# Performance work log

Measured on AMD Instinct MI355X. Metric: run time of the kernel, lower is better.

Reference implementation:

```python
import jax, jax.numpy as jnp
import numpy as np
import math

HIDDEN = 768
LABEL_NUM = 16
N_HEADS = 12
HEAD_DIM = HIDDEN // N_HEADS


def setup_inputs() -> dict:
    key = jax.random.key(0)
    ks = jax.random.split(key, 8)
    B, S, L, Ls, H = 8, 128, LABEL_NUM, 8, HIDDEN
    std = 1.0 / math.sqrt(H)
    return {
        "token_embs": jax.random.normal(ks[0], (B, S, H), jnp.float32),
        "label_embs": jax.random.normal(ks[1], (L, Ls, H), jnp.float32),
        "token_mask": jnp.ones((B, S), jnp.float32),
        "label_mask": jnp.ones((L, Ls), jnp.float32),
        "Wq": jax.random.normal(ks[2], (H, H), jnp.float32) * std,
        "bq": jnp.zeros((H,), jnp.float32),
        "Wk": jax.random.normal(ks[3], (H, H), jnp.float32) * std,
        "bk": jnp.zeros((H,), jnp.float32),
        "Wv": jax.random.normal(ks[4], (H, H), jnp.float32) * std,
        "bv": jnp.zeros((H,), jnp.float32),
    }


def reference(token_embs, label_embs, token_mask, label_mask, Wq, bq, Wk, bk, Wv, bv):
    B, S, H = token_embs.shape
    L, Ls, _ = label_embs.shape
    T = S + Ls
    # broadcast (instead of repeat) then concat: [B, L, T, H] -> [B*L, T, H]
    tok = jnp.broadcast_to(token_embs[:, None, :, :], (B, L, S, H))
    lab = jnp.broadcast_to(label_embs[None, :, :, :], (B, L, Ls, H))
    x = jnp.concatenate([tok, lab], axis=2).reshape(B * L, T, H)
    # mask: [B*L, T]; extended additive mask (1-m)*-10000
    tm = jnp.broadcast_to(token_mask[:, None, :], (B, L, S))
    lm = jnp.broadcast_to(label_mask[None, :, :], (B, L, Ls))
    mask = jnp.concatenate([tm, lm], axis=2).reshape(B * L, T)
    bias = (1.0 - mask) * -10000.0  # [BL, T]
    # QKV (torch Linear: y = x W^T + b)
    q = (x @ Wq.T + bq).reshape(B * L, T, N_HEADS, HEAD_DIM)
    k = (x @ Wk.T + bk).reshape(B * L, T, N_HEADS, HEAD_DIM)
    v = (x @ Wv.T + bv).reshape(B * L, T, N_HEADS, HEAD_DIM)
    scores = jnp.einsum("bthd,bshd->bhts", q, k) / math.sqrt(HEAD_DIM)
    scores = scores + bias[:, None, None, :]
    probs = jax.nn.softmax(scores, axis=-1)
    ctx = jnp.einsum("bhts,bshd->bthd", probs, v).reshape(B * L, T, H)
    # [B, L, T, H] -> [B, T, L, H]
    fused = ctx.reshape(B, L, T, H).transpose(0, 2, 1, 3)
    return (fused,)
```

## Files before the change

kernel.cpp:

```cpp
#include <hip/hip_runtime.h>
#include <hip/hip_bf16.h>
#include <stdint.h>

#define HIDDEN 768
#define NH 12
#define HD 64
#define BB 8
#define SS 128
#define LL 16
#define LS 8
#define TT 136
#define NROWS 1152
#define BH (BB * NH)

typedef __attribute__((ext_vector_type(8))) short bf16x8;
typedef __attribute__((ext_vector_type(4))) float f32x4;
typedef __hip_bfloat16 bf16;

__device__ inline float tof(bf16 x) { return __bfloat162float(x); }
__device__ inline uint16_t b16bits(float f) {
    bf16 h = __float2bfloat16(f);
    union { bf16 h; uint16_t u; } u; u.h = h; return u.u;
}

__global__ __launch_bounds__(256) void qkv_kernel(
    const float* __restrict__ tok, const float* __restrict__ lab,
    const float* __restrict__ Wq, const float* __restrict__ bq,
    const float* __restrict__ Wk, const float* __restrict__ bk,
    const float* __restrict__ Wv, const float* __restrict__ bv,
    bf16* __restrict__ Qw, bf16* __restrict__ Kw, bf16* __restrict__ Vw)
{
    __shared__ __align__(16) uint16_t As[64 * 40];
    __shared__ __align__(16) uint16_t Bs[128 * 40];

    int tid = threadIdx.x;
    int lane = tid & 63, wv = tid >> 6;
    int ml = lane & 15, quad = lane >> 4;
    int mt = blockIdx.x / 18, nt = blockIdx.x % 18;
    int wr = wv >> 1, wc = wv & 1;

    int mat = nt / 6;
    int col0 = (nt % 6) * 128;
    const float* wbase = (mat == 0) ? Wq : ((mat == 1) ? Wk : Wv);
    const float* bptr  = (mat == 0) ? bq : ((mat == 1) ? bk : bv);
    bf16* obase        = (mat == 0) ? Qw : ((mat == 1) ? Kw : Vw);

    int ar0 = mt * 64;
    const float* asrc = (ar0 < 1024) ? (tok + (size_t)ar0 * HIDDEN)
                                     : (lab + (size_t)(ar0 - 1024) * HIDDEN);
    const float* bsrc = wbase + (size_t)col0 * HIDDEN;

    f32x4 acc[2][4] = {};

    for (int k0 = 0; k0 < HIDDEN; k0 += 32) {
        #pragma unroll
        for (int i = 0; i < 2; ++i) {
            int gi = i * 256 + tid;
            int r = gi >> 3, kc = (gi & 7) * 4;
            float4 v = *reinterpret_cast<const float4*>(asrc + (size_t)r * HIDDEN + k0 + kc);
            ushort4 hh;
            hh.x = b16bits(v.x); hh.y = b16bits(v.y);
            hh.z = b16bits(v.z); hh.w = b16bits(v.w);
            *reinterpret_cast<ushort4*>(&As[r * 40 + kc]) = hh;
        }
        #pragma unroll
        for (int i = 0; i < 4; ++i) {
            int gi = i * 256 + tid;
            int r = gi >> 3, kc = (gi & 7) * 4;
            float4 v = *reinterpret_cast<const float4*>(bsrc + (size_t)r * HIDDEN + k0 + kc);
            ushort4 hh;
            hh.x = b16bits(v.x); hh.y = b16bits(v.y);
            hh.z = b16bits(v.z); hh.w = b16bits(v.w);
            *reinterpret_cast<ushort4*>(&Bs[r * 40 + kc]) = hh;
        }
        __syncthreads();

        bf16x8 af[2], bfr[4];
        #pragma unroll
        for (int rt = 0; rt < 2; ++rt)
            af[rt] = *reinterpret_cast<const bf16x8*>(&As[(wr * 32 + rt * 16 + ml) * 40 + quad * 8]);
        #pragma unroll
        for (int ct = 0; ct < 4; ++ct)
            bfr[ct] = *reinterpret_cast<const bf16x8*>(&Bs[(wc * 64 + ct * 16 + ml) * 40 + quad * 8]);
        #pragma unroll
        for (int rt = 0; rt < 2; ++rt)
            #pragma unroll
            for (int ct = 0; ct < 4; ++ct)
                acc[rt][ct] = __builtin_amdgcn_mfma_f32_16x16x32_bf16(af[rt], bfr[ct], acc[rt][ct], 0, 0, 0);
        __syncthreads();
    }

    #pragma unroll
    for (int ct = 0; ct < 4; ++ct) {
        int c = col0 + wc * 64 + ct * 16 + ml;
        float bvv = bptr[c];
        #pragma unroll
        for (int rt = 0; rt < 2; ++rt) {
            #pragma unroll
            for (int reg = 0; reg < 4; ++reg) {
                int R = mt * 64 + wr * 32 + rt * 16 + quad * 4 + reg;
                obase[(size_t)R * HIDDEN + c] = __float2bfloat16(acc[rt][ct][reg] + bvv);
            }
        }
    }
}

__global__ __launch_bounds__(256) void attn_tt_kernel(
    const bf16* __restrict__ Qw, const bf16* __restrict__ Kw,
    const bf16* __restrict__ Vw, const float* __restrict__ tmask,
    bf16* __restrict__ ctx_tt, float* __restrict__ m_tt, float* __restrict__ d_tt)
{
    __shared__ __align__(16) uint32_t KldsW[128 * 36];
    __shared__ __align__(16) uint32_t VtW[64 * 68];
    __shared__ __align__(16) uint32_t PW[4][16 * 68];
    __shared__ float bias_s[128];

    int bh = blockIdx.x >> 1;
    int hf = blockIdx.x & 1;
    int b = bh / NH, h = bh % NH;
    int tid = threadIdx.x;
    int lane = tid & 63, wv = tid >> 6;
    int ml = lane & 15, quad = lane >> 4;

    for (int i = tid; i < 128 * 32; i += 256) {
        int s = i >> 5, w = i & 31;
        KldsW[s * 36 + w] =
            reinterpret_cast<const uint32_t*>(Kw + (size_t)(b * SS + s) * HIDDEN + h * HD)[w];
    }
    for (int i = tid; i < 64 * 64; i += 256) {
        int d = i & 63, s2 = i >> 6;
        const uint16_t* v0 = reinterpret_cast<const uint16_t*>(Vw + (size_t)(b * SS + 2 * s2) * HIDDEN + h * HD);
        const uint16_t* v1 = reinterpret_cast<const uint16_t*>(Vw + (size_t)(b * SS + 2 * s2 + 1) * HIDDEN + h * HD);
        VtW[d * 68 + s2] = (uint32_t)v0[d] | ((uint32_t)v1[d] << 16);
    }
    for (int i = tid; i < 128; i += 256)
        bias_s[i] = (1.0f - tmask[b * SS + i]) * -10000.0f;
    __syncthreads();

    const bf16* Klb = reinterpret_cast<const bf16*>(KldsW);
    const bf16* Vtb = reinterpret_cast<const bf16*>(VtW);
    const bf16* Pb  = reinterpret_cast<const bf16*>(PW[wv]);

    int qr = hf * 64 + wv * 16 + ml;
    const bf16* qp = Qw + (size_t)(b * SS + qr) * HIDDEN + h * HD + quad * 8;
    bf16x8 a0 = *reinterpret_cast<const bf16x8*>(qp);
    bf16x8 a1 = *reinterpret_cast<const bf16x8*>(qp + 32);

    f32x4 sc[8];
    #pragma unroll
    for (int ct = 0; ct < 8; ++ct) {
        const bf16* kp = Klb + (ct * 16 + ml) * 72 + quad * 8;
        bf16x8 b0 = *reinterpret_cast<const bf16x8*>(kp);
        bf16x8 b1 = *reinterpret_cast<const bf16x8*>(kp + 32);
        f32x4 z = {0.f, 0.f, 0.f, 0.f};
        z = __builtin_amdgcn_mfma_f32_16x16x32_bf16(a0, b0, z, 0, 0, 0);
        z = __builtin_amdgcn_mfma_f32_16x16x32_bf16(a1, b1, z, 0, 0, 0);
        sc[ct] = z;
    }

    float mx[4] = {-1e30f, -1e30f, -1e30f, -1e30f};
    #pragma unroll
    for (int ct = 0; ct < 8; ++ct) {
        float bc = bias_s[ct * 16 + ml];
        #pragma unroll
        for (int reg = 0; reg < 4; ++reg) {
            float v = sc[ct][reg] * 0.125f + bc;
            sc[ct][reg] = v;
            mx[reg] = fmaxf(mx[reg], v);
        }
    }
    #pragma unroll
    for (int reg = 0; reg < 4; ++reg)
        #pragma unroll
        for (int off = 1; off < 16; off <<= 1)
            mx[reg] = fmaxf(mx[reg], __shfl_xor(mx[reg], off));

    float Zs[4] = {0.f, 0.f, 0.f, 0.f};
    #pragma unroll
    for (int ct = 0; ct < 8; ++ct) {
        #pragma unroll
        for (int reg = 0; reg < 4; ++reg) {
            float e = __expf(sc[ct][reg] - mx[reg]);
            sc[ct][reg] = e;
            Zs[reg] += e;
        }
    }
    #pragma unroll
    for (int reg = 0; reg < 4; ++reg)
        #pragma unroll
        for (int off = 1; off < 16; off <<= 1)
            Zs[reg] += __shfl_xor(Zs[reg], off);

    #pragma unroll
    for (int reg = 0; reg < 4; ++reg) {
        int gr = bh * 128 + hf * 64 + wv * 16 + quad * 4 + reg;
        if (ml == 0) { m_tt[gr] = mx[reg]; d_tt[gr] = Zs[reg]; }
    }

    #pragma unroll
    for (int ct = 0; ct < 8; ++ct) {
        #pragma unroll
        for (int reg = 0; reg < 4; ++reg) {
            float e = sc[ct][reg];
            float ep = __shfl_xor(e, 1);
            if ((ml & 1) == 0)
                PW[wv][(quad * 4 + reg) * 68 + ct * 8 + (ml >> 1)] =
                    (uint32_t)b16bits(e) | ((uint32_t)b16bits(ep) << 16);
        }
    }

    float rZ[4];
    #pragma unroll
    for (int reg = 0; reg < 4; ++reg) rZ[reg] = 1.0f / Zs[reg];

    #pragma unroll
    for (int ct4 = 0; ct4 < 4; ++ct4) {
        f32x4 acc = {0.f, 0.f, 0.f, 0.f};
        #pragma unroll
        for (int ks = 0; ks < 4; ++ks) {
            bf16x8 ap = *reinterpret_cast<const bf16x8*>(Pb + ml * 136 + ks * 32 + quad * 8);
            bf16x8 bp = *reinterpret_cast<const bf16x8*>(Vtb + (ct4 * 16 + ml) * 136 + ks * 32 + quad * 8);
            acc = __builtin_amdgcn_mfma_f32_16x16x32_bf16(ap, bp, acc, 0, 0, 0);
        }
        #pragma unroll
        for (int reg = 0; reg < 4; ++reg) {
            int gr = bh * 128 + hf * 64 + wv * 16 + quad * 4 + reg;
            ctx_tt[(size_t)gr * 64 + ct4 * 16 + ml] = __float2bfloat16(acc[reg] * rZ[reg]);
        }
    }
}

__global__ __launch_bounds__(256) void attn_merge_kernel(
    const bf16* __restrict__ Qw, const bf16* __restrict__ Kw,
    const bf16* __restrict__ Vw,
    const bf16* __restrict__ ctx_tt, const float* __restrict__ m_tt,
    const float* __restrict__ d_tt,
    const float* __restrict__ tmask, const float* __restrict__ lmask,
    float* __restrict__ out)
{
    __shared__ __align__(16) uint32_t VtW[64 * 84];
    __shared__ __align__(16) uint32_t PW[4][16 * 84];
    __shared__ float mtt_s[128], dtt_s[128], bias_t[128];
    __shared__ float bias_l[16];

    int p = blockIdx.x & 7;
    int h = (blockIdx.x >> 3) % NH;
    int b = blockIdx.x / (8 * NH);
    int l0 = 2 * p, l1 = l0 + 1;
    int bh = b * NH + h;
    int tid = threadIdx.x;
    int lane = tid & 63, wv = tid >> 6;
    int ml = lane & 15, quad = lane >> 4;

    for (int i = tid; i < 64 * 80; i += 256) {
        int d = i & 63, s2 = i >> 6;
        uint32_t w = 0;
        #pragma unroll
        for (int half = 0; half < 2; ++half) {
            int s = 2 * s2 + half;
            int row = -1;
            if (s < 128)      row = b * SS + s;
            else if (s < 136) row = 1024 + l0 * LS + (s - 128);
            else if (s < 144) row = 1024 + l1 * LS + (s - 136);
            uint16_t v = 0;
            if (row >= 0)
                v = reinterpret_cast<const uint16_t*>(Vw + (size_t)row * HIDDEN + h * HD)[d];
            w |= (uint32_t)v << (16 * half);
        }
        VtW[d * 84 + s2] = w;
    }
    if (tid < 128) {
        mtt_s[tid] = m_tt[bh * 128 + tid];
        dtt_s[tid] = d_tt[bh * 128 + tid];
        bias_t[tid] = (1.0f - tmask[b * SS + tid]) * -10000.0f;
    }
    if (tid < 16) {
        int labk = (tid < 8) ? (l0 * LS + tid) : (l1 * LS + tid - 8);
        bias_l[tid] = (1.0f - lmask[labk]) * -10000.0f;
    }
    for (int i = tid; i < 4 * 16 * 8; i += 256) {
        int wvb = i >> 7, rem = i & 127;
        PW[wvb][(rem >> 3) * 84 + 72 + (rem & 7)] = 0;
    }
    __syncthreads();

    const bf16* Vtb = reinterpret_cast<const bf16*>(VtW);
    const bf16* Pb  = reinterpret_cast<const bf16*>(PW[wv]);
    const bf16x8 zfrag = {0, 0, 0, 0, 0, 0, 0, 0};

    int kprow = 1024 + ((ml < 8) ? (l0 * LS + ml) : (l1 * LS + ml - 8));
    const bf16* kpp = Kw + (size_t)kprow * HIDDEN + h * HD + quad * 8;
    bf16x8 kb0 = *reinterpret_cast<const bf16x8*>(kpp);
    bf16x8 kb1 = *reinterpret_cast<const bf16x8*>(kpp + 32);

    for (int rt = wv; rt < 8; rt += 4) {
        int tq = rt * 16 + ml;
        const bf16* qp = Qw + (size_t)(b * SS + tq) * HIDDEN + h * HD + quad * 8;
        bf16x8 a0 = *reinterpret_cast<const bf16x8*>(qp);
        bf16x8 a1 = *reinterpret_cast<const bf16x8*>(qp + 32);

        f32x4 z = {0.f, 0.f, 0.f, 0.f};
        z = __builtin_amdgcn_mfma_f32_16x16x32_bf16(a0, kb0, z, 0, 0, 0);
        z = __builtin_amdgcn_mfma_f32_16x16x32_bf16(a1, kb1, z, 0, 0, 0);

        float w0r[4], i0r[4], w1r[4], i1r[4];
        #pragma unroll
        for (int reg = 0; reg < 4; ++reg) {
            int grow = rt * 16 + quad * 4 + reg;
            float s = z[reg] * 0.125f + bias_l[ml];
            float m = s;
            m = fmaxf(m, __shfl_xor(m, 1));
            m = fmaxf(m, __shfl_xor(m, 2));
            m = fmaxf(m, __shfl_xor(m, 4));
            float mtt = mtt_s[grow], dtt = dtt_s[grow];
            float m_new = fmaxf(mtt, m);
            float e = __expf(s - m_new);
            float dh = e;
            dh += __shfl_xor(dh, 1);
            dh += __shfl_xor(dh, 2);
            dh += __shfl_xor(dh, 4);
            float alpha = __expf(mtt - m_new);
            float w = alpha * dtt;
            float inv = 1.0f / (w + dh);
            w0r[reg] = __shfl(w,   (lane & 48));
            i0r[reg] = __shfl(inv, (lane & 48));
            w1r[reg] = __shfl(w,   (lane & 48) | 8);
            i1r[reg] = __shfl(inv, (lane & 48) | 8);
            float ep = __shfl_xor(e, 1);
            if ((ml & 1) == 0)
                PW[wv][(quad * 4 + reg) * 84 + (ml >> 1)] =
                    (uint32_t)b16bits(e) | ((uint32_t)b16bits(ep) << 16);
        }

        bf16x8 aP0 = (quad == 0) ? *reinterpret_cast<const bf16x8*>(Pb + ml * 168)     : zfrag;
        bf16x8 aP1 = (quad == 0) ? *reinterpret_cast<const bf16x8*>(Pb + ml * 168 + 8) : zfrag;
        #pragma unroll
        for (int ct4 = 0; ct4 < 4; ++ct4) {
            const bf16* vrow = Vtb + (ct4 * 16 + ml) * 168;
            bf16x8 bV0 = (quad == 0) ? *reinterpret_cast<const bf16x8*>(vrow + 128) : zfrag;
            bf16x8 bV1 = (quad == 0) ? *reinterpret_cast<const bf16x8*>(vrow + 136) : zfrag;
            f32x4 pv0 = {0.f, 0.f, 0.f, 0.f}, pv1 = {0.f, 0.f, 0.f, 0.f};
            pv0 = __builtin_amdgcn_mfma_f32_16x16x32_bf16(aP0, bV0, pv0, 0, 0, 0);
            pv1 = __builtin_amdgcn_mfma_f32_16x16x32_bf16(aP1, bV1, pv1, 0, 0, 0);
            #pragma unroll
            for (int reg = 0; reg < 4; ++reg) {
                int grow = rt * 16 + quad * 4 + reg;
                float c = tof(ctx_tt[(size_t)(bh * 128 + grow) * 64 + ct4 * 16 + ml]);
                size_t ob = (((size_t)b * TT + grow) * LL) * HIDDEN + h * HD + ct4 * 16 + ml;
                out[ob + (size_t)l0 * HIDDEN] = (w0r[reg] * c + pv0[reg]) * i0r[reg];
                out[ob + (size_t)l1 * HIDDEN] = (w1r[reg] * c + pv1[reg]) * i1r[reg];
            }
        }
    }

    if (wv == 3) {
        int qrow = 1024 + ((ml < 8) ? (l0 * LS + ml) : (l1 * LS + ml - 8));
        const bf16* qp = Qw + (size_t)qrow * HIDDEN + h * HD + quad * 8;
        bf16x8 a0 = *reinterpret_cast<const bf16x8*>(qp);
        bf16x8 a1 = *reinterpret_cast<const bf16x8*>(qp + 32);

        f32x4 sc[9];
        #pragma unroll
        for (int ct = 0; ct < 9; ++ct) {
            bf16x8 b0, b1;
            if (ct < 8) {
                const bf16* kp = Kw + (size_t)(b * SS + ct * 16 + ml) * HIDDEN + h * HD + quad * 8;
                b0 = *reinterpret_cast<const bf16x8*>(kp);
                b1 = *reinterpret_cast<const bf16x8*>(kp + 32);
            } else { b0 = kb0; b1 = kb1; }
            f32x4 zz = {0.f, 0.f, 0.f, 0.f};
            zz = __builtin_amdgcn_mfma_f32_16x16x32_bf16(a0, b0, zz, 0, 0, 0);
            zz = __builtin_amdgcn_mfma_f32_16x16x32_bf16(a1, b1, zz, 0, 0, 0);
            sc[ct] = zz;
        }

        float mx[4] = {-1e30f, -1e30f, -1e30f, -1e30f};
        #pragma unroll
        for (int ct = 0; ct < 9; ++ct) {
            #pragma unroll
            for (int reg = 0; reg < 4; ++reg) {
                int rq = quad * 4 + reg;
                float bc = (ct < 8) ? bias_t[ct * 16 + ml]
                                    : (((rq < 8) != (ml < 8)) ? -1e30f : bias_l[ml]);
                float v = sc[ct][reg] * 0.125f + bc;
                sc[ct][reg] = v;
                mx[reg] = fmaxf(mx[reg], v);
            }
        }
        #pragma unroll
        for (int reg = 0; reg < 4; ++reg)
            #pragma unroll
            for (int off = 1; off < 16; off <<= 1)
                mx[reg] = fmaxf(mx[reg], __shfl_xor(mx[reg], off));

        float Zs[4] = {0.f, 0.f, 0.f, 0.f};
        #pragma unroll
        for (int ct = 0; ct < 9; ++ct) {
            #pragma unroll
            for (int reg = 0; reg < 4; ++reg) {
                float e = __expf(sc[ct][reg] - mx[reg]);
                sc[ct][reg] = e;
                Zs[reg] += e;
            }
        }
        #pragma unroll
        for (int reg = 0; reg < 4; ++reg)
            #pragma unroll
            for (int off = 1; off < 16; off <<= 1)
                Zs[reg] += __shfl_xor(Zs[reg], off);
        float zi[4];
        #pragma unroll
        for (int reg = 0; reg < 4; ++reg) zi[reg] = 1.0f / Zs[reg];

        #pragma unroll
        for (int ct = 0; ct < 9; ++ct) {
            #pragma unroll
            for (int reg = 0; reg < 4; ++reg) {
                float e = sc[ct][reg];
                float ep = __shfl_xor(e, 1);
                if ((ml & 1) == 0)
                    PW[wv][(quad * 4 + reg) * 84 + ct * 8 + (ml >> 1)] =
                        (uint32_t)b16bits(e) | ((uint32_t)b16bits(ep) << 16);
            }
        }

        #pragma unroll
        for (int ct4 = 0; ct4 < 4; ++ct4) {
            f32x4 acc = {0.f, 0.f, 0.f, 0.f};
            #pragma unroll
            for (int ks = 0; ks < 5; ++ks) {
                bf16x8 ap = *reinterpret_cast<const bf16x8*>(Pb + ml * 168 + ks * 32 + quad * 8);
                bf16x8 bp = *reinterpret_cast<const bf16x8*>(Vtb + (ct4 * 16 + ml) * 168 + ks * 32 + quad * 8);
                acc = __builtin_amdgcn_mfma_f32_16x16x32_bf16(ap, bp, acc, 0, 0, 0);
            }
            #pragma unroll
            for (int reg = 0; reg < 4; ++reg) {
                int rq = quad * 4 + reg;
                int l = (rq < 8) ? l0 : l1;
                int t = SS + (rq & 7);
                out[(((size_t)b * TT + t) * LL + l) * HIDDEN + h * HD + ct4 * 16 + ml] =
                    acc[reg] * zi[reg];
            }
        }
    }
}

extern "C" void kernel_launch(void* const* d_in, const int* in_sizes, int n_in,
                              void* d_out, int out_size, void* d_ws, size_t ws_size,
                              hipStream_t stream)
{
    const float* tok   = (const float*)d_in[0];
    const float* lab   = (const float*)d_in[1];
    const float* tmask = (const float*)d_in[2];
    const float* lmask = (const float*)d_in[3];
    const float* Wq    = (const float*)d_in[4];
    const float* bq    = (const float*)d_in[5];
    const float* Wk    = (const float*)d_in[6];
    const float* bk    = (const float*)d_in[7];
    const float* Wv    = (const float*)d_in[8];
    const float* bv    = (const float*)d_in[9];

    bf16* Qw = (bf16*)d_ws;
    bf16* Kw = Qw + (size_t)NROWS * HIDDEN;
    bf16* Vw = Kw + (size_t)NROWS * HIDDEN;
    bf16* ctx = Vw + (size_t)NROWS * HIDDEN;
    float* m_tt = (float*)(ctx + (size_t)BH * 128 * 64);
    float* d_tt = m_tt + BH * 128;

    qkv_kernel<<<dim3(18 * 18), 256, 0, stream>>>(
        tok, lab, Wq, bq, Wk, bk, Wv, bv, Qw, Kw, Vw);
    attn_tt_kernel<<<dim3(BH * 2), 256, 0, stream>>>(
        Qw, Kw, Vw, tmask, ctx, m_tt, d_tt);
    attn_merge_kernel<<<dim3(BB * NH * 8), 256, 0, stream>>>(
        Qw, Kw, Vw, ctx, m_tt, d_tt, tmask, lmask, (float*)d_out);
}
```

Measured before the change: 149.6 us.

## Double-buffer QKV GEMM loads and use 32x32 MFMA for merge PV

```diff
diff --git a/kernel.cpp b/kernel.cpp
--- a/kernel.cpp
+++ b/kernel.cpp
@@ -15,6 +15,7 @@
 
 typedef __attribute__((ext_vector_type(8))) short bf16x8;
 typedef __attribute__((ext_vector_type(4))) float f32x4;
+typedef __attribute__((ext_vector_type(16))) float f32x16;
 typedef __hip_bfloat16 bf16;
 
 __device__ inline float tof(bf16 x) { return __bfloat162float(x); }
@@ -30,8 +31,8 @@
     const float* __restrict__ Wv, const float* __restrict__ bv,
     bf16* __restrict__ Qw, bf16* __restrict__ Kw, bf16* __restrict__ Vw)
 {
-    __shared__ __align__(16) uint16_t As[64 * 40];
-    __shared__ __align__(16) uint16_t Bs[128 * 40];
+    __shared__ __align__(16) uint16_t As[2][64 * 40];
+    __shared__ __align__(16) uint16_t Bs[2][128 * 40];
 
     int tid = threadIdx.x;
     int lane = tid & 63, wv = tid >> 6;
@@ -50,44 +51,62 @@
                                      : (lab + (size_t)(ar0 - 1024) * HIDDEN);
     const float* bsrc = wbase + (size_t)col0 * HIDDEN;
 
+    int ra_r[2], ra_c[2], rb_r[4], rb_c[4];
+    #pragma unroll
+    for (int i = 0; i < 2; ++i) { int gi = i * 256 + tid; ra_r[i] = gi >> 3; ra_c[i] = (gi & 7) * 4; }
+    #pragma unroll
+    for (int i = 0; i < 4; ++i) { int gi = i * 256 + tid; rb_r[i] = gi >> 3; rb_c[i] = (gi & 7) * 4; }
+
+    float4 ra[2], rb[4];
+    #pragma unroll
+    for (int i = 0; i < 2; ++i)
+        ra[i] = *reinterpret_cast<const float4*>(asrc + (size_t)ra_r[i] * HIDDEN + ra_c[i]);
+    #pragma unroll
+    for (int i = 0; i < 4; ++i)
+        rb[i] = *reinterpret_cast<const float4*>(bsrc + (size_t)rb_r[i] * HIDDEN + rb_c[i]);
+
     f32x4 acc[2][4] = {};
+    int p = 0;
 
     for (int k0 = 0; k0 < HIDDEN; k0 += 32) {
         #pragma unroll
         for (int i = 0; i < 2; ++i) {
-            int gi = i * 256 + tid;
-            int r = gi >> 3, kc = (gi & 7) * 4;
-            float4 v = *reinterpret_cast<const float4*>(asrc + (size_t)r * HIDDEN + k0 + kc);
             ushort4 hh;
-            hh.x = b16bits(v.x); hh.y = b16bits(v.y);
-            hh.z = b16bits(v.z); hh.w = b16bits(v.w);
-            *reinterpret_cast<ushort4*>(&As[r * 40 + kc]) = hh;
+            hh.x = b16bits(ra[i].x); hh.y = b16bits(ra[i].y);
+            hh.z = b16bits(ra[i].z); hh.w = b16bits(ra[i].w);
+            *reinterpret_cast<ushort4*>(&As[p][ra_r[i] * 40 + ra_c[i]]) = hh;
         }
         #pragma unroll
         for (int i = 0; i < 4; ++i) {
-            int gi = i * 256 + tid;
-            int r = gi >> 3, kc = (gi & 7) * 4;
-            float4 v = *reinterpret_cast<const float4*>(bsrc + (size_t)r * HIDDEN + k0 + kc);
             ushort4 hh;
-            hh.x = b16bits(v.x); hh.y = b16bits(v.y);
-            hh.z = b16bits(v.z); hh.w = b16bits(v.w);
-            *reinterpret_cast<ushort4*>(&Bs[r * 40 + kc]) = hh;
+            hh.x = b16bits(rb[i].x); hh.y = b16bits(rb[i].y);
+            hh.z = b16bits(rb[i].z); hh.w = b16bits(rb[i].w);
+            *reinterpret_cast<ushort4*>(&Bs[p][rb_r[i] * 40 + rb_c[i]]) = hh;
         }
         __syncthreads();
 
+        if (k0 + 32 < HIDDEN) {
+            #pragma unroll
+            for (int i = 0; i < 2; ++i)
+                ra[i] = *reinterpret_cast<const float4*>(asrc + (size_t)ra_r[i] * HIDDEN + k0 + 32 + ra_c[i]);
+            #pragma unroll
+            for (int i = 0; i < 4; ++i)
+                rb[i] = *reinterpret_cast<const float4*>(bsrc + (size_t)rb_r[i] * HIDDEN + k0 + 32 + rb_c[i]);
+        }
+
         bf16x8 af[2], bfr[4];
         #pragma unroll
         for (int rt = 0; rt < 2; ++rt)
-            af[rt] = *reinterpret_cast<const bf16x8*>(&As[(wr * 32 + rt * 16 + ml) * 40 + quad * 8]);
+            af[rt] = *reinterpret_cast<const bf16x8*>(&As[p][(wr * 32 + rt * 16 + ml) * 40 + quad * 8]);
         #pragma unroll
         for (int ct = 0; ct < 4; ++ct)
-            bfr[ct] = *reinterpret_cast<const bf16x8*>(&Bs[(wc * 64 + ct * 16 + ml) * 40 + quad * 8]);
+            bfr[ct] = *reinterpret_cast<const bf16x8*>(&Bs[p][(wc * 64 + ct * 16 + ml) * 40 + quad * 8]);
         #pragma unroll
         for (int rt = 0; rt < 2; ++rt)
             #pragma unroll
             for (int ct = 0; ct < 4; ++ct)
                 acc[rt][ct] = __builtin_amdgcn_mfma_f32_16x16x32_bf16(af[rt], bfr[ct], acc[rt][ct], 0, 0, 0);
-        __syncthreads();
+        p ^= 1;
     }
 
     #pragma unroll
@@ -239,7 +258,9 @@
     float* __restrict__ out)
 {
     __shared__ __align__(16) uint32_t VtW[64 * 84];
-    __shared__ __align__(16) uint32_t PW[4][16 * 84];
+    __shared__ __align__(16) uint32_t PWL[16 * 84];
+    __shared__ __align__(16) uint32_t P2W[4][32 * 8];
+    __shared__ float wtab[4][32], itab[4][32];
     __shared__ float mtt_s[128], dtt_s[128], bias_t[128];
     __shared__ float bias_l[16];
 
@@ -251,6 +272,7 @@
     int tid = threadIdx.x;
     int lane = tid & 63, wv = tid >> 6;
     int ml = lane & 15, quad = lane >> 4;
+    int hl = lane & 31, hi = lane >> 5;
 
     for (int i = tid; i < 64 * 80; i += 256) {
         int d = i & 63, s2 = i >> 6;
@@ -278,82 +300,87 @@
         int labk = (tid < 8) ? (l0 * LS + tid) : (l1 * LS + tid - 8);
         bias_l[tid] = (1.0f - lmask[labk]) * -10000.0f;
     }
-    for (int i = tid; i < 4 * 16 * 8; i += 256) {
-        int wvb = i >> 7, rem = i & 127;
-        PW[wvb][(rem >> 3) * 84 + 72 + (rem & 7)] = 0;
-    }
+    if (tid < 128)
+        PWL[(tid >> 3) * 84 + 72 + (tid & 7)] = 0;
     __syncthreads();
 
     const bf16* Vtb = reinterpret_cast<const bf16*>(VtW);
-    const bf16* Pb  = reinterpret_cast<const bf16*>(PW[wv]);
-    const bf16x8 zfrag = {0, 0, 0, 0, 0, 0, 0, 0};
 
     int kprow = 1024 + ((ml < 8) ? (l0 * LS + ml) : (l1 * LS + ml - 8));
     const bf16* kpp = Kw + (size_t)kprow * HIDDEN + h * HD + quad * 8;
     bf16x8 kb0 = *reinterpret_cast<const bf16x8*>(kpp);
     bf16x8 kb1 = *reinterpret_cast<const bf16x8*>(kpp + 32);
 
-    for (int rt = wv; rt < 8; rt += 4) {
-        int tq = rt * 16 + ml;
-        const bf16* qp = Qw + (size_t)(b * SS + tq) * HIDDEN + h * HD + quad * 8;
-        bf16x8 a0 = *reinterpret_cast<const bf16x8*>(qp);
-        bf16x8 a1 = *reinterpret_cast<const bf16x8*>(qp + 32);
-
-        f32x4 z = {0.f, 0.f, 0.f, 0.f};
-        z = __builtin_amdgcn_mfma_f32_16x16x32_bf16(a0, kb0, z, 0, 0, 0);
-        z = __builtin_amdgcn_mfma_f32_16x16x32_bf16(a1, kb1, z, 0, 0, 0);
-
-        float w0r[4], i0r[4], w1r[4], i1r[4];
-        #pragma unroll
-        for (int reg = 0; reg < 4; ++reg) {
-            int grow = rt * 16 + quad * 4 + reg;
-            float s = z[reg] * 0.125f + bias_l[ml];
-            float m = s;
-            m = fmaxf(m, __shfl_xor(m, 1));
-            m = fmaxf(m, __shfl_xor(m, 2));
-            m = fmaxf(m, __shfl_xor(m, 4));
-            float mtt = mtt_s[grow], dtt = dtt_s[grow];
-            float m_new = fmaxf(mtt, m);
-            float e = __expf(s - m_new);
-            float dh = e;
-            dh += __shfl_xor(dh, 1);
-            dh += __shfl_xor(dh, 2);
-            dh += __shfl_xor(dh, 4);
-            float alpha = __expf(mtt - m_new);
-            float w = alpha * dtt;
-            float inv = 1.0f / (w + dh);
-            w0r[reg] = __shfl(w,   (lane & 48));
-            i0r[reg] = __shfl(inv, (lane & 48));
-            w1r[reg] = __shfl(w,   (lane & 48) | 8);
-            i1r[reg] = __shfl(inv, (lane & 48) | 8);
-            float ep = __shfl_xor(e, 1);
-            if ((ml & 1) == 0)
-                PW[wv][(quad * 4 + reg) * 84 + (ml >> 1)] =
-                    (uint32_t)b16bits(e) | ((uint32_t)b16bits(ep) << 16);
-        }
-
-        bf16x8 aP0 = (quad == 0) ? *reinterpret_cast<const bf16x8*>(Pb + ml * 168)     : zfrag;
-        bf16x8 aP1 = (quad == 0) ? *reinterpret_cast<const bf16x8*>(Pb + ml * 168 + 8) : zfrag;
-        #pragma unroll
-        for (int ct4 = 0; ct4 < 4; ++ct4) {
-            const bf16* vrow = Vtb + (ct4 * 16 + ml) * 168;
-            bf16x8 bV0 = (quad == 0) ? *reinterpret_cast<const bf16x8*>(vrow + 128) : zfrag;
-            bf16x8 bV1 = (quad == 0) ? *reinterpret_cast<const bf16x8*>(vrow + 136) : zfrag;
-            f32x4 pv0 = {0.f, 0.f, 0.f, 0.f}, pv1 = {0.f, 0.f, 0.f, 0.f};
-            pv0 = __builtin_amdgcn_mfma_f32_16x16x32_bf16(aP0, bV0, pv0, 0, 0, 0);
-            pv1 = __builtin_amdgcn_mfma_f32_16x16x32_bf16(aP1, bV1, pv1, 0, 0, 0);
+    if (wv < 3) {
+        const bf16* P2b = reinterpret_cast<const bf16*>(P2W[wv]);
+        for (int rt = wv; rt < 8; rt += 3) {
+            int tq = rt * 16 + ml;
+            const bf16* qp = Qw + (size_t)(b * SS + tq) * HIDDEN + h * HD + quad * 8;
+            bf16x8 a0 = *reinterpret_cast<const bf16x8*>(qp);
+            bf16x8 a1 = *reinterpret_cast<const bf16x8*>(qp + 32);
+
+            f32x4 z = {0.f, 0.f, 0.f, 0.f};
+            z = __builtin_amdgcn_mfma_f32_16x16x32_bf16(a0, kb0, z, 0, 0, 0);
+            z = __builtin_amdgcn_mfma_f32_16x16x32_bf16(a1, kb1, z, 0, 0, 0);
+
             #pragma unroll
             for (int reg = 0; reg < 4; ++reg) {
-                int grow = rt * 16 + quad * 4 + reg;
-                float c = tof(ctx_tt[(size_t)(bh * 128 + grow) * 64 + ct4 * 16 + ml]);
-                size_t ob = (((size_t)b * TT + grow) * LL) * HIDDEN + h * HD + ct4 * 16 + ml;
-                out[ob + (size_t)l0 * HIDDEN] = (w0r[reg] * c + pv0[reg]) * i0r[reg];
-                out[ob + (size_t)l1 * HIDDEN] = (w1r[reg] * c + pv1[reg]) * i1r[reg];
-            }
-        }
-    }
-
-    if (wv == 3) {
+                int trow = quad * 4 + reg;
+                float s = z[reg] * 0.125f + bias_l[ml];
+                float m = s;
+                m = fmaxf(m, __shfl_xor(m, 1));
+                m = fmaxf(m, __shfl_xor(m, 2));
+                m = fmaxf(m, __shfl_xor(m, 4));
+                float mtt = mtt_s[rt * 16 + trow], dtt = dtt_s[rt * 16 + trow];
+                float m_new = fmaxf(mtt, m);
+                float e = __expf(s - m_new);
+                float dh = e;
+                dh += __shfl_xor(dh, 1);
+                dh += __shfl_xor(dh, 2);
+                dh += __shfl_xor(dh, 4);
+                float alpha = __expf(mtt - m_new);
+                float w = alpha * dtt;
+                float inv = 1.0f / (w + dh);
+                if (ml == 0) { wtab[wv][trow] = w;      itab[wv][trow] = inv; }
+                if (ml == 8) { wtab[wv][16 + trow] = w; itab[wv][16 + trow] = inv; }
+                float ep = __shfl_xor(e, 1);
+                if ((ml & 1) == 0) {
+                    uint32_t pk = (uint32_t)b16bits(e) | ((uint32_t)b16bits(ep) << 16);
+                    P2W[wv][trow * 8 + (ml >> 1)]        = (ml < 8) ? pk : 0u;
+                    P2W[wv][(16 + trow) * 8 + (ml >> 1)] = (ml < 8) ? 0u : pk;
+                }
+            }
+
+            bf16x8 ap  = *reinterpret_cast<const bf16x8*>(P2b + hl * 16 + hi * 8);
+            bf16x8 bv0 = *reinterpret_cast<const bf16x8*>(Vtb + hl * 168 + 128 + hi * 8);
+            bf16x8 bv1 = *reinterpret_cast<const bf16x8*>(Vtb + (32 + hl) * 168 + 128 + hi * 8);
+            f32x16 c0 = {}, c1 = {};
+            c0 = __builtin_amdgcn_mfma_f32_32x32x16_bf16(ap, bv0, c0, 0, 0, 0);
+            c1 = __builtin_amdgcn_mfma_f32_32x32x16_bf16(ap, bv1, c1, 0, 0, 0);
+
+            float cv0[8], cv1[8];
+            #pragma unroll
+            for (int reg = 0; reg < 8; ++reg) {
+                int row = (reg & 3) + 8 * (reg >> 2) + 4 * hi;
+                const bf16* cp = ctx_tt + (size_t)(bh * 128 + rt * 16 + row) * 64;
+                cv0[reg] = tof(cp[hl]);
+                cv1[reg] = tof(cp[32 + hl]);
+            }
+            #pragma unroll
+            for (int reg = 0; reg < 16; ++reg) {
+                int row = (reg & 3) + 8 * (reg >> 2) + 4 * hi;
+                int trow = row & 15;
+                int lsel = (row < 16) ? l0 : l1;
+                float w = wtab[wv][row], inv = itab[wv][row];
+                float c0v = (reg < 8) ? cv0[reg] : cv0[reg - 8];
+                float c1v = (reg < 8) ? cv1[reg] : cv1[reg - 8];
+                size_t ob = (((size_t)b * TT + rt * 16 + trow) * LL + lsel) * HIDDEN + h * HD;
+                out[ob + hl]      = (w * c0v + c0[reg]) * inv;
+                out[ob + 32 + hl] = (w * c1v + c1[reg]) * inv;
+            }
+        }
+    } else {
+        const bf16* Pb = reinterpret_cast<const bf16*>(PWL);
         int qrow = 1024 + ((ml < 8) ? (l0 * LS + ml) : (l1 * LS + ml - 8));
         const bf16* qp = Qw + (size_t)qrow * HIDDEN + h * HD + quad * 8;
         bf16x8 a0 = *reinterpret_cast<const bf16x8*>(qp);
@@ -419,7 +446,7 @@
                 float e = sc[ct][reg];
                 float ep = __shfl_xor(e, 1);
                 if ((ml & 1) == 0)
-                    PW[wv][(quad * 4 + reg) * 84 + ct * 8 + (ml >> 1)] =
+                    PWL[(quad * 4 + reg) * 84 + ct * 8 + (ml >> 1)] =
                         (uint32_t)b16bits(e) | ((uint32_t)b16bits(ep) << 16);
             }
         }
```

Result: faster. 138.2 us (-7.6%).
